# Optimization experiments

Measured on AMD Instinct MI355X. Metric: run time of the kernel, lower is better.

The kernel has to match this reference:

```python
import jax, jax.numpy as jnp
import numpy as np

N_NEURONS = 1024
TABLE_SIZE = 65536  # array_size (2048 quotients) * 2**remainder_size (32)
BATCH = 8192


def setup_inputs() -> dict:
    key = jax.random.key(0)
    k1, k2 = jax.random.split(key)
    # Input tuples: one fingerprint per neuron per sample, value = (quotient << rs) | remainder
    data = jax.random.randint(k1, (BATCH, N_NEURONS), 0, TABLE_SIZE, dtype=jnp.int32)
    # Dense membership/counter table equivalent to the fitted quotient filter state
    # (quotient filter with full remainders stored is an exact fingerprint set).
    table = jax.random.uniform(k2, (N_NEURONS, TABLE_SIZE), dtype=jnp.float32)
    return {"data": data, "table": table}


def reference(data, table):
    # check_member(neuron=j, quotient=data[i,j]>>rs, remainder=data[i,j]&mask)
    # == table[j, data[i,j]]; multi_rank sums memberships over neurons.
    neuron_idx = jnp.arange(table.shape[0])[None, :]          # [1, N]
    gathered = table[neuron_idx, data]                        # [B, N] gather
    response = jnp.sum(gathered, axis=1)                      # [B]
    return response
```

## Files before the change

kernel.cpp:

```cpp
#include <hip/hip_runtime.h>

#define N_NEURONS 1024
#define TABLE_SIZE 65536
#define BATCH 8192
#define NGROUPS 8
#define NPG 128
#define SPB 128
#define NCHUNK 8
#define TS ((size_t)TABLE_SIZE)

__global__ __launch_bounds__(256) void qw_partial_kernel(
    const int* __restrict__ data,
    const float* __restrict__ table,
    float* __restrict__ part)
{
    const int b      = blockIdx.x;
    const int g      = b & (NGROUPS - 1);
    const int sub    = b >> 3;
    const int t      = threadIdx.x;
    const int h      = t & 1;
    const int sid    = t >> 1;
    const int sample = sub * SPB + sid;

    const int* __restrict__ dptr =
        data + (size_t)sample * N_NEURONS + g * NPG + h * 8;
    const float* __restrict__ tb =
        table + (size_t)(g * NPG + h * 8) * TABLE_SIZE;

#define IDX(c)  (*reinterpret_cast<const int4*>(dptr + (c) * 16))
#define IDX2(c) (*reinterpret_cast<const int4*>(dptr + (c) * 16 + 4))

#define GATHER(d0,d1,d2,d3,d4,d5,d6,d7, c, I0, I1)                    \
    d0 = tb[((size_t)(c) * 16 + 0) * TS + (size_t)(I0).x];            \
    d1 = tb[((size_t)(c) * 16 + 1) * TS + (size_t)(I0).y];            \
    d2 = tb[((size_t)(c) * 16 + 2) * TS + (size_t)(I0).z];            \
    d3 = tb[((size_t)(c) * 16 + 3) * TS + (size_t)(I0).w];            \
    d4 = tb[((size_t)(c) * 16 + 4) * TS + (size_t)(I1).x];            \
    d5 = tb[((size_t)(c) * 16 + 5) * TS + (size_t)(I1).y];            \
    d6 = tb[((size_t)(c) * 16 + 6) * TS + (size_t)(I1).z];            \
    d7 = tb[((size_t)(c) * 16 + 7) * TS + (size_t)(I1).w];

#define SUM8(d0,d1,d2,d3,d4,d5,d6,d7) \
    (((d0 + d1) + (d2 + d3)) + ((d4 + d5) + (d6 + d7)))

    int4 p0 = IDX(0), p1 = IDX2(0);
    int4 q0 = IDX(1), q1 = IDX2(1);

    float A0,A1,A2,A3,A4,A5,A6,A7;
    float B0,B1,B2,B3,B4,B5,B6,B7;
    float acc = 0.0f;

    GATHER(A0,A1,A2,A3,A4,A5,A6,A7, 0, p0, p1);

    GATHER(B0,B1,B2,B3,B4,B5,B6,B7, 1, q0, q1);
    p0 = IDX(2); p1 = IDX2(2);
    __builtin_amdgcn_s_barrier();
    acc += SUM8(A0,A1,A2,A3,A4,A5,A6,A7);

    GATHER(A0,A1,A2,A3,A4,A5,A6,A7, 2, p0, p1);
    q0 = IDX(3); q1 = IDX2(3);
    __builtin_amdgcn_s_barrier();
    acc += SUM8(B0,B1,B2,B3,B4,B5,B6,B7);

    GATHER(B0,B1,B2,B3,B4,B5,B6,B7, 3, q0, q1);
    p0 = IDX(4); p1 = IDX2(4);
    __builtin_amdgcn_s_barrier();
    acc += SUM8(A0,A1,A2,A3,A4,A5,A6,A7);

    GATHER(A0,A1,A2,A3,A4,A5,A6,A7, 4, p0, p1);
    q0 = IDX(5); q1 = IDX2(5);
    __builtin_amdgcn_s_barrier();
    acc += SUM8(B0,B1,B2,B3,B4,B5,B6,B7);

    GATHER(B0,B1,B2,B3,B4,B5,B6,B7, 5, q0, q1);
    p0 = IDX(6); p1 = IDX2(6);
    __builtin_amdgcn_s_barrier();
    acc += SUM8(A0,A1,A2,A3,A4,A5,A6,A7);

    GATHER(A0,A1,A2,A3,A4,A5,A6,A7, 6, p0, p1);
    q0 = IDX(7); q1 = IDX2(7);
    __builtin_amdgcn_s_barrier();
    acc += SUM8(B0,B1,B2,B3,B4,B5,B6,B7);

    GATHER(B0,B1,B2,B3,B4,B5,B6,B7, 7, q0, q1);
    __builtin_amdgcn_s_barrier();
    acc += SUM8(A0,A1,A2,A3,A4,A5,A6,A7);

    acc += SUM8(B0,B1,B2,B3,B4,B5,B6,B7);

#undef GATHER
#undef SUM8
#undef IDX
#undef IDX2

    acc += __shfl_xor(acc, 1, 64);
    if (h == 0) {
        part[(size_t)g * BATCH + sample] = acc;
    }
}

__global__ __launch_bounds__(256) void qw_reduce_kernel(
    const float* __restrict__ part,
    float* __restrict__ out)
{
    const int i = blockIdx.x * 256 + threadIdx.x;
    float s = 0.0f;
#pragma unroll
    for (int g = 0; g < NGROUPS; ++g) {
        s += part[(size_t)g * BATCH + i];
    }
    out[i] = s;
}

__global__ __launch_bounds__(256) void qw_gather_kernel(
    const int* __restrict__ data,
    const float* __restrict__ table,
    float* __restrict__ out)
{
    const int gtid   = blockIdx.x * blockDim.x + threadIdx.x;
    const int sample = gtid >> 6;
    const int lane   = threadIdx.x & 63;
    if (sample >= BATCH) return;
    const int* __restrict__ row = data + (size_t)sample * N_NEURONS;
    float acc = 0.0f;
#pragma unroll
    for (int k = 0; k < 4; ++k) {
        const int jb = 256 * k + 4 * lane;
        const int4 idx4 = *reinterpret_cast<const int4*>(row + jb);
        acc += table[(size_t)(jb + 0) * TABLE_SIZE + idx4.x];
        acc += table[(size_t)(jb + 1) * TABLE_SIZE + idx4.y];
        acc += table[(size_t)(jb + 2) * TABLE_SIZE + idx4.z];
        acc += table[(size_t)(jb + 3) * TABLE_SIZE + idx4.w];
    }
#pragma unroll
    for (int off = 32; off >= 1; off >>= 1) acc += __shfl_xor(acc, off, 64);
    if (lane == 0) out[sample] = acc;
}

extern "C" void kernel_launch(void* const* d_in, const int* in_sizes, int n_in,
                              void* d_out, int out_size, void* d_ws, size_t ws_size,
                              hipStream_t stream)
{
    const int*   data  = (const int*)d_in[0];
    const float* table = (const float*)d_in[1];
    float*       out   = (float*)d_out;

    const size_t need = (size_t)NGROUPS * BATCH * sizeof(float);
    if (ws_size >= need) {
        float* part = (float*)d_ws;
        const int blocks = (BATCH / SPB) * NGROUPS;
        qw_partial_kernel<<<blocks, 256, 0, stream>>>(data, table, part);
        qw_reduce_kernel<<<BATCH / 256, 256, 0, stream>>>(part, out);
    } else {
        qw_gather_kernel<<<BATCH / 4, 256, 0, stream>>>(data, table, out);
    }
}
```

Measured before the change: 84.17 us.

## Pace neuron-group blocks in lockstep with global atomic barriers per chunk

Doubles samples per block (512 threads, 256 samples) and inserts a per-group global barrier: after each chunk, all blocks of a neuron group increment an atomic counter and spin, with a bounded budget, until every block arrives. The intent is to keep blocks of a group working on the same 16-neuron table rows together, so the gathered table slices stay resident in cache. A small init kernel zeroes the counters on every launch. Spin-waiting adds latency and relies on co-residency of the group's blocks, and the timeout budget keeps it from deadlocking.

```diff
diff --git a/kernel.cpp b/kernel.cpp
--- a/kernel.cpp
+++ b/kernel.cpp
@@ -5,14 +5,22 @@
 #define BATCH 8192
 #define NGROUPS 8
 #define NPG 128
-#define SPB 128
+#define SPB 256
+#define TPB 512
 #define NCHUNK 8
+#define NBLK ((BATCH / SPB) * NGROUPS)
+#define BPG (NBLK / NGROUPS)
 #define TS ((size_t)TABLE_SIZE)
 
-__global__ __launch_bounds__(256) void qw_partial_kernel(
+__global__ void qw_init_kernel(unsigned* __restrict__ bar) {
+    bar[threadIdx.x] = 0u;
+}
+
+__global__ __launch_bounds__(TPB) void qw_partial_kernel(
     const int* __restrict__ data,
     const float* __restrict__ table,
-    float* __restrict__ part)
+    float* __restrict__ part,
+    unsigned* __restrict__ bar)
 {
     const int b      = blockIdx.x;
     const int g      = b & (NGROUPS - 1);
@@ -26,6 +34,7 @@
         data + (size_t)sample * N_NEURONS + g * NPG + h * 8;
     const float* __restrict__ tb =
         table + (size_t)(g * NPG + h * 8) * TABLE_SIZE;
+    unsigned* __restrict__ gbar = bar + g * 32;
 
 #define IDX(c)  (*reinterpret_cast<const int4*>(dptr + (c) * 16))
 #define IDX2(c) (*reinterpret_cast<const int4*>(dptr + (c) * 16 + 4))
@@ -43,51 +52,67 @@
 #define SUM8(d0,d1,d2,d3,d4,d5,d6,d7) \
     (((d0 + d1) + (d2 + d3)) + ((d4 + d5) + (d6 + d7)))
 
+#define PACE(c)                                                            \
+    asm volatile("" ::: "memory");                                         \
+    __builtin_amdgcn_s_barrier();                                          \
+    if (t == 0) {                                                          \
+        __hip_atomic_fetch_add(&gbar[c], 1u, __ATOMIC_RELAXED,             \
+                               __HIP_MEMORY_SCOPE_AGENT);                  \
+        int budget = 20000;                                                \
+        while (__hip_atomic_load(&gbar[c], __ATOMIC_RELAXED,               \
+                                 __HIP_MEMORY_SCOPE_AGENT) < (unsigned)BPG \
+               && --budget) {                                              \
+            __builtin_amdgcn_s_sleep(1);                                   \
+        }                                                                  \
+    }                                                                      \
+    __builtin_amdgcn_s_barrier();                                          \
+    asm volatile("" ::: "memory");
+
     int4 p0 = IDX(0), p1 = IDX2(0);
-    int4 q0 = IDX(1), q1 = IDX2(1);
-
     float A0,A1,A2,A3,A4,A5,A6,A7;
     float B0,B1,B2,B3,B4,B5,B6,B7;
     float acc = 0.0f;
 
     GATHER(A0,A1,A2,A3,A4,A5,A6,A7, 0, p0, p1);
+    int4 q0 = IDX(1), q1 = IDX2(1);
 
     GATHER(B0,B1,B2,B3,B4,B5,B6,B7, 1, q0, q1);
     p0 = IDX(2); p1 = IDX2(2);
-    __builtin_amdgcn_s_barrier();
+    PACE(0);
     acc += SUM8(A0,A1,A2,A3,A4,A5,A6,A7);
 
     GATHER(A0,A1,A2,A3,A4,A5,A6,A7, 2, p0, p1);
     q0 = IDX(3); q1 = IDX2(3);
-    __builtin_amdgcn_s_barrier();
+    PACE(1);
     acc += SUM8(B0,B1,B2,B3,B4,B5,B6,B7);
 
     GATHER(B0,B1,B2,B3,B4,B5,B6,B7, 3, q0, q1);
     p0 = IDX(4); p1 = IDX2(4);
-    __builtin_amdgcn_s_barrier();
+    PACE(2);
     acc += SUM8(A0,A1,A2,A3,A4,A5,A6,A7);
 
     GATHER(A0,A1,A2,A3,A4,A5,A6,A7, 4, p0, p1);
     q0 = IDX(5); q1 = IDX2(5);
-    __builtin_amdgcn_s_barrier();
+    PACE(3);
     acc += SUM8(B0,B1,B2,B3,B4,B5,B6,B7);
 
     GATHER(B0,B1,B2,B3,B4,B5,B6,B7, 5, q0, q1);
     p0 = IDX(6); p1 = IDX2(6);
-    __builtin_amdgcn_s_barrier();
+    PACE(4);
     acc += SUM8(A0,A1,A2,A3,A4,A5,A6,A7);
 
     GATHER(A0,A1,A2,A3,A4,A5,A6,A7, 6, p0, p1);
     q0 = IDX(7); q1 = IDX2(7);
-    __builtin_amdgcn_s_barrier();
+    PACE(5);
     acc += SUM8(B0,B1,B2,B3,B4,B5,B6,B7);
 
     GATHER(B0,B1,B2,B3,B4,B5,B6,B7, 7, q0, q1);
-    __builtin_amdgcn_s_barrier();
+    PACE(6);
     acc += SUM8(A0,A1,A2,A3,A4,A5,A6,A7);
 
     acc += SUM8(B0,B1,B2,B3,B4,B5,B6,B7);
 
+#undef PACE
 #undef GATHER
 #undef SUM8
 #undef IDX
@@ -127,10 +152,10 @@
     for (int k = 0; k < 4; ++k) {
         const int jb = 256 * k + 4 * lane;
         const int4 idx4 = *reinterpret_cast<const int4*>(row + jb);
-        acc += table[(size_t)(jb + 0) * TABLE_SIZE + idx4.x];
-        acc += table[(size_t)(jb + 1) * TABLE_SIZE + idx4.y];
-        acc += table[(size_t)(jb + 2) * TABLE_SIZE + idx4.z];
-        acc += table[(size_t)(jb + 3) * TABLE_SIZE + idx4.w];
+        acc += table[(size_t)(jb + 0) * TS + idx4.x];
+        acc += table[(size_t)(jb + 1) * TS + idx4.y];
+        acc += table[(size_t)(jb + 2) * TS + idx4.z];
+        acc += table[(size_t)(jb + 3) * TS + idx4.w];
     }
 #pragma unroll
     for (int off = 32; off >= 1; off >>= 1) acc += __shfl_xor(acc, off, 64);
@@ -145,11 +170,13 @@
     const float* table = (const float*)d_in[1];
     float*       out   = (float*)d_out;
 
-    const size_t need = (size_t)NGROUPS * BATCH * sizeof(float);
-    if (ws_size >= need) {
-        float* part = (float*)d_ws;
-        const int blocks = (BATCH / SPB) * NGROUPS;
-        qw_partial_kernel<<<blocks, 256, 0, stream>>>(data, table, part);
+    const size_t part_bytes = (size_t)NGROUPS * BATCH * sizeof(float);
+    const size_t bar_bytes  = (size_t)NGROUPS * 32 * sizeof(unsigned);
+    if (ws_size >= part_bytes + bar_bytes) {
+        float*    part = (float*)d_ws;
+        unsigned* bar  = (unsigned*)((char*)d_ws + part_bytes);
+        qw_init_kernel<<<1, NGROUPS * 32, 0, stream>>>(bar);
+        qw_partial_kernel<<<NBLK, TPB, 0, stream>>>(data, table, part, bar);
         qw_reduce_kernel<<<BATCH / 256, 256, 0, stream>>>(part, out);
     } else {
         qw_gather_kernel<<<BATCH / 4, 256, 0, stream>>>(data, table, out);
```

After: 104.6 us. 24.3% more time.
